# Performance work log

Measured on AMD Instinct MI355X. Metric: run time of the kernel, lower is better.

Reference implementation:

```python
import jax, jax.numpy as jnp
import numpy as np

KSIZE = 51  # radius=50 is even -> incremented to 51 in __init__


def _gaussian_1d(ksize):
    # cv2.getGaussianKernel with sigma<=0: sigma = 0.3*((ksize-1)*0.5 - 1) + 0.8
    sigma = 0.3 * ((ksize - 1) * 0.5 - 1) + 0.8
    x = np.arange(ksize, dtype=np.float64) - (ksize - 1) / 2
    g = np.exp(-(x * x) / (2.0 * sigma * sigma))
    g = g / g.sum()
    return g.astype(np.float32)


def _blur(img, kernel1d):
    """Separable Gaussian blur with reflect padding.
    Mathematically identical to the 2D conv with outer(g, g) in the torch code.
    img: (b, c, h, w), kernel1d: (k,)
    """
    k = kernel1d.shape[0]
    p = k // 2
    b, c, h, w = img.shape
    x = jnp.pad(img, ((0, 0), (0, 0), (p, p), (p, p)), mode='reflect')
    x = x.reshape(b * c, 1, h + 2 * p, w + 2 * p)
    # vertical pass then horizontal pass (conv vs correlation irrelevant: symmetric kernel)
    kv = kernel1d.reshape(1, 1, k, 1)
    kh = kernel1d.reshape(1, 1, 1, k)
    dn = ('NCHW', 'OIHW', 'NCHW')
    x = jax.lax.conv_general_dilated(x, kv, (1, 1), 'VALID', dimension_numbers=dn)
    x = jax.lax.conv_general_dilated(x, kh, (1, 1), 'VALID', dimension_numbers=dn)
    return x.reshape(b, c, h, w)


def setup_inputs() -> dict:
    key = jax.random.key(0)
    img = jax.random.uniform(key, (16, 3, 512, 512), dtype=jnp.float32)
    kernel1d = jnp.asarray(_gaussian_1d(KSIZE))
    return {"img": img, "kernel1d": kernel1d}


def reference(img, kernel1d):
    weight = 0.5
    threshold = 10.0
    blur = _blur(img, kernel1d)
    residual = img - blur
    mask = (jnp.abs(residual) * 255.0 > threshold).astype(img.dtype)
    soft_mask = _blur(mask, kernel1d)
    sharp = jnp.clip(img + weight * residual, 0.0, 1.0)
    return soft_mask * sharp + (1.0 - soft_mask) * img
```

## Files before the change

### kernel.cpp

```cpp
#include <hip/hip_runtime.h>
#include <hip/hip_bf16.h>


typedef __attribute__((ext_vector_type(8))) short bf16x8;
typedef __attribute__((ext_vector_type(4))) float f32x4;

constexpr int IMG = 512, NIMG = 48, K = 51;
constexpr int SP = 136;
constexpr int YP = 136;
constexpr int SROWS = 128;
constexpr int SDATA = 122;

__device__ __forceinline__ float bf2f(unsigned short u) {
    return __builtin_bit_cast(float, (unsigned)u << 16);
}
__device__ __forceinline__ unsigned short f2bf(float f) {
    unsigned u = __builtin_bit_cast(unsigned, f);
    u += 0x7FFF + ((u >> 16) & 1);
    return (unsigned short)(u >> 16);
}
__device__ __forceinline__ int refl(int i) {
    i = i < 0 ? -i : i;
    return i >= IMG ? 2 * IMG - 2 - i : i;
}

template <int PASS>
__global__ __launch_bounds__(512, 6) void usm_kern(const float* __restrict__ img,
                                                   unsigned short* __restrict__ resbuf,
                                                   unsigned char* __restrict__ maskbuf,
                                                   float* __restrict__ out,
                                                   const float* __restrict__ k1d) {
    __shared__ unsigned short st[SROWS * SP];
    __shared__ unsigned short Hl[64 * YP];

    const int tid = threadIdx.x, lane = tid & 63;
    const int wv = __builtin_amdgcn_readfirstlane(tid >> 6);
    const int m16 = lane & 15, g = lane >> 4;

    const int id = blockIdx.x;
    const int sw = (id & 7) * 384 + (id >> 3);
    const int bz = sw >> 6, r6 = sw & 63, byy = r6 >> 3, bxx = r6 & 7;
    const int x0 = bxx * 64, y0 = byy * 64;
    const size_t base = (size_t)bz * (IMG * IMG);
    const float* __restrict__ imgb = img + base;
    unsigned short* __restrict__ resb = resbuf + base;
    unsigned char* __restrict__ maskb = maskbuf + base;
    float* __restrict__ outb = out + base;

    bf16x8 a_v[2], a_h[2];
#pragma unroll
    for (int rs = 0; rs < 2; ++rs) {
        float gt[9];
#pragma unroll
        for (int e = 0; e < 9; ++e) {
            const int t = 32 * rs + 8 * g + e - m16;
            gt[e] = ((unsigned)t < (unsigned)K) ? k1d[t] : 0.f;
        }
#pragma unroll
        for (int j = 0; j < 8; ++j) {
            a_v[rs][j] = (short)f2bf(gt[j]);
            a_h[rs][j] = (short)f2bf(gt[j + 1]);
        }
    }
    const float gg0 = k1d[0], gg49 = k1d[49], gg50 = k1d[50];

    const bool xedge = (bxx == 0) | (bxx == 7);
    const int r0t = tid >> 4, c8 = (tid & 15) * 8;
#pragma unroll
    for (int j = 0; j < 4; ++j) {
        const int s = r0t + 32 * j;
        const int rowo = refl(y0 - 33 + min(s, SDATA - 1)) * IMG + (x0 - 32 + c8);
        unsigned pk[4];
        if (PASS == 0) {
            float v[8];
            if (!xedge) {
                const f32x4 f0 = *(const f32x4*)&imgb[rowo];
                const f32x4 f1 = *(const f32x4*)&imgb[rowo + 4];
#pragma unroll
                for (int e = 0; e < 4; ++e) { v[e] = f0[e]; v[e + 4] = f1[e]; }
            } else {
                const int rb = rowo - (x0 - 32 + c8);
#pragma unroll
                for (int e = 0; e < 8; ++e) v[e] = imgb[rb + refl(x0 - 32 + c8 + e)];
            }
#pragma unroll
            for (int w = 0; w < 4; ++w)
                pk[w] = (unsigned)f2bf(v[2 * w]) | ((unsigned)f2bf(v[2 * w + 1]) << 16);
        } else {
            unsigned char mb[8];
            if (!xedge) {
                const uint2 mv = *(const uint2*)&maskb[rowo];
#pragma unroll
                for (int e = 0; e < 4; ++e) {
                    mb[e] = (unsigned char)(mv.x >> (8 * e));
                    mb[e + 4] = (unsigned char)(mv.y >> (8 * e));
                }
            } else {
                const int rb = rowo - (x0 - 32 + c8);
#pragma unroll
                for (int e = 0; e < 8; ++e) mb[e] = maskb[rb + refl(x0 - 32 + c8 + e)];
            }
#pragma unroll
            for (int w = 0; w < 4; ++w)
                pk[w] = (mb[2 * w] ? 0x3F80u : 0u) | ((mb[2 * w + 1] ? 0x3F80u : 0u) << 16);
        }
        *(uint4*)&st[s * SP + c8] = make_uint4(pk[0], pk[1], pk[2], pk[3]);
    }

    f32x4 ivp[2];
    uint2 rvp[2];
#pragma unroll
    for (int k2 = 0; k2 < 2; ++k2) {
        const int t = wv + 8 * k2;
        const int xs = t & 3, ys = t >> 2;
        const int di = (y0 + 16 * ys + m16) * IMG + (x0 + 16 * xs + 4 * g);
        ivp[k2] = *(const f32x4*)&imgb[di];
        if (PASS == 1) rvp[k2] = *(const uint2*)&resb[di];
    }
    __syncthreads();

#pragma unroll
    for (int k4 = 0; k4 < 4; ++k4) {
        const int t = wv + 8 * k4;
        const int xs = t & 3, yt = t >> 2;
        f32x4 acc = {0.f, 0.f, 0.f, 0.f};
#pragma unroll
        for (int rs = 0; rs < 2; ++rs) {
            const bf16x8 ad = *(const bf16x8*)&st[(16 * yt + m16) * SP + 16 * xs + 8 + 32 * rs + 8 * g];
            acc = __builtin_amdgcn_mfma_f32_16x16x32_bf16(ad, a_h[rs], acc, 0, 0, 0);
        }
        if (m16 == 0) {
#pragma unroll
            for (int q = 0; q < 4; ++q)
                acc[q] = fmaf(gg0, bf2f(st[(16 * yt + 4 * g + q) * SP + 16 * xs + 7]), acc[q]);
        }
        if (m16 == 15) {
#pragma unroll
            for (int q = 0; q < 4; ++q)
                acc[q] = fmaf(gg50, bf2f(st[(16 * yt + 4 * g + q) * SP + 16 * xs + 72]), acc[q]);
        }
        const unsigned lo = (unsigned)f2bf(acc[0]) | ((unsigned)f2bf(acc[1]) << 16);
        const unsigned hi = (unsigned)f2bf(acc[2]) | ((unsigned)f2bf(acc[3]) << 16);
        *(uint2*)&Hl[(16 * xs + m16) * YP + 16 * yt + 4 * g] = make_uint2(lo, hi);
    }
    __syncthreads();

#pragma unroll
    for (int k2 = 0; k2 < 2; ++k2) {
        const int t = wv + 8 * k2;
        const int xs = t & 3, ys = t >> 2;
        f32x4 acc = {0.f, 0.f, 0.f, 0.f};
#pragma unroll
        for (int rs = 0; rs < 2; ++rs) {
            const bf16x8 ah = *(const bf16x8*)&Hl[(16 * xs + m16) * YP + 16 * ys + 8 + 32 * rs + 8 * g];
            acc = __builtin_amdgcn_mfma_f32_16x16x32_bf16(ah, a_v[rs], acc, 0, 0, 0);
        }
        if (m16 == 14) {
#pragma unroll
            for (int q = 0; q < 4; ++q)
                acc[q] = fmaf(gg50, bf2f(Hl[(16 * xs + 4 * g + q) * YP + 16 * ys + 72]), acc[q]);
        }
        if (m16 == 15) {
#pragma unroll
            for (int q = 0; q < 4; ++q) {
                const int hb = (16 * xs + 4 * g + q) * YP + 16 * ys;
                acc[q] = fmaf(gg49, bf2f(Hl[hb + 72]), fmaf(gg50, bf2f(Hl[hb + 73]), acc[q]));
            }
        }
        const int di = (y0 + 16 * ys + m16) * IMG + (x0 + 16 * xs + 4 * g);
        const f32x4 iv = ivp[k2];
        if (PASS == 0) {
            unsigned mw = 0;
            unsigned rp[2];
            float rv[4];
#pragma unroll
            for (int q = 0; q < 4; ++q) {
                rv[q] = iv[q] - acc[q];
                mw |= (fabsf(rv[q]) * 255.0f > 10.0f ? 1u : 0u) << (8 * q);
            }
            rp[0] = (unsigned)f2bf(rv[0]) | ((unsigned)f2bf(rv[1]) << 16);
            rp[1] = (unsigned)f2bf(rv[2]) | ((unsigned)f2bf(rv[3]) << 16);
            *(uint2*)&resb[di] = make_uint2(rp[0], rp[1]);
            *(unsigned*)&maskb[di] = mw;
        } else {
            f32x4 o;
#pragma unroll
            for (int q = 0; q < 4; ++q) {
                const unsigned rw = (q < 2) ? rvp[k2].x : rvp[k2].y;
                const float rvq = bf2f((unsigned short)(rw >> ((q & 1) * 16)));
                float sharp = fmaf(0.5f, rvq, iv[q]);
                sharp = fminf(fmaxf(sharp, 0.f), 1.f);
                o[q] = fmaf(acc[q], sharp - iv[q], iv[q]);
            }
            *(f32x4*)&outb[di] = o;
        }
    }
}

extern "C" void kernel_launch(void* const* d_in, const int* in_sizes, int n_in,
                              void* d_out, int out_size, void* d_ws, size_t ws_size,
                              hipStream_t stream) {
    (void)in_sizes; (void)n_in; (void)out_size; (void)ws_size;
    const float* img = (const float*)d_in[0];
    const float* k1d = (const float*)d_in[1];
    float* out = (float*)d_out;
    unsigned short* rs = (unsigned short*)d_ws;
    unsigned char* mk = (unsigned char*)d_ws + (size_t)NIMG * IMG * IMG * 2;

    const dim3 grid(NIMG * 64);

    usm_kern<0><<<grid, 512, 0, stream>>>(img, rs, mk, out, k1d);
    usm_kern<1><<<grid, 512, 0, stream>>>(img, rs, mk, out, k1d);
}
```

Baseline: 113.1 us.

## Drop mask buffer, derive mask from bf16 residual, alias LDS tiles

Pass 0 no longer writes a separate byte mask. Pass 1 reads the bf16 residual halo and rebuilds the mask with an integer magnitude compare, which removes one global buffer write and read. The horizontal-pass LDS buffer now reuses the staging buffer, with an extra barrier, so LDS use shrinks and launch bounds rise to 8 blocks. Manual bf16 rounding is replaced by the packed v_cvt_pk_bf16_f32 instruction, and the MFMA operands are swapped so edge taps need fewer lanes. The risk is that the threshold test on a bf16-rounded residual can flip mask bits near the cutoff, and the transposed Hl writes become scalar 16-bit LDS stores.

Result: no change. 113.5 us (+0.3%).

```diff
diff --git a/kernel.cpp b/kernel.cpp
--- a/kernel.cpp
+++ b/kernel.cpp
@@ -14,10 +14,10 @@
 __device__ __forceinline__ float bf2f(unsigned short u) {
     return __builtin_bit_cast(float, (unsigned)u << 16);
 }
-__device__ __forceinline__ unsigned short f2bf(float f) {
-    unsigned u = __builtin_bit_cast(unsigned, f);
-    u += 0x7FFF + ((u >> 16) & 1);
-    return (unsigned short)(u >> 16);
+__device__ __forceinline__ unsigned cvtpk(float lo, float hi) {
+    unsigned r;
+    asm("v_cvt_pk_bf16_f32 %0, %1, %2" : "=v"(r) : "v"(lo), "v"(hi));
+    return r;
 }
 __device__ __forceinline__ int refl(int i) {
     i = i < 0 ? -i : i;
@@ -25,13 +25,12 @@
 }
 
 template <int PASS>
-__global__ __launch_bounds__(512, 6) void usm_kern(const float* __restrict__ img,
+__global__ __launch_bounds__(512, 8) void usm_kern(const float* __restrict__ img,
                                                    unsigned short* __restrict__ resbuf,
-                                                   unsigned char* __restrict__ maskbuf,
                                                    float* __restrict__ out,
                                                    const float* __restrict__ k1d) {
     __shared__ unsigned short st[SROWS * SP];
-    __shared__ unsigned short Hl[64 * YP];
+    unsigned short* const Hl = st;
 
     const int tid = threadIdx.x, lane = tid & 63;
     const int wv = __builtin_amdgcn_readfirstlane(tid >> 6);
@@ -44,7 +43,6 @@
     const size_t base = (size_t)bz * (IMG * IMG);
     const float* __restrict__ imgb = img + base;
     unsigned short* __restrict__ resb = resbuf + base;
-    unsigned char* __restrict__ maskb = maskbuf + base;
     float* __restrict__ outb = out + base;
 
     bf16x8 a_v[2], a_h[2];
@@ -56,11 +54,13 @@
             const int t = 32 * rs + 8 * g + e - m16;
             gt[e] = ((unsigned)t < (unsigned)K) ? k1d[t] : 0.f;
         }
-#pragma unroll
-        for (int j = 0; j < 8; ++j) {
-            a_v[rs][j] = (short)f2bf(gt[j]);
-            a_h[rs][j] = (short)f2bf(gt[j + 1]);
-        }
+        uint4 uv, uh;
+        uv.x = cvtpk(gt[0], gt[1]); uv.y = cvtpk(gt[2], gt[3]);
+        uv.z = cvtpk(gt[4], gt[5]); uv.w = cvtpk(gt[6], gt[7]);
+        uh.x = cvtpk(gt[1], gt[2]); uh.y = cvtpk(gt[3], gt[4]);
+        uh.z = cvtpk(gt[5], gt[6]); uh.w = cvtpk(gt[7], gt[8]);
+        a_v[rs] = __builtin_bit_cast(bf16x8, uv);
+        a_h[rs] = __builtin_bit_cast(bf16x8, uh);
     }
     const float gg0 = k1d[0], gg49 = k1d[49], gg50 = k1d[50];
 
@@ -84,25 +84,27 @@
                 for (int e = 0; e < 8; ++e) v[e] = imgb[rb + refl(x0 - 32 + c8 + e)];
             }
 #pragma unroll
-            for (int w = 0; w < 4; ++w)
-                pk[w] = (unsigned)f2bf(v[2 * w]) | ((unsigned)f2bf(v[2 * w + 1]) << 16);
+            for (int w = 0; w < 4; ++w) pk[w] = cvtpk(v[2 * w], v[2 * w + 1]);
         } else {
-            unsigned char mb[8];
+            unsigned rw[4];
             if (!xedge) {
-                const uint2 mv = *(const uint2*)&maskb[rowo];
-#pragma unroll
-                for (int e = 0; e < 4; ++e) {
-                    mb[e] = (unsigned char)(mv.x >> (8 * e));
-                    mb[e + 4] = (unsigned char)(mv.y >> (8 * e));
-                }
+                const uint4 q4 = *(const uint4*)&resb[rowo];
+                rw[0] = q4.x; rw[1] = q4.y; rw[2] = q4.z; rw[3] = q4.w;
             } else {
                 const int rb = rowo - (x0 - 32 + c8);
 #pragma unroll
-                for (int e = 0; e < 8; ++e) mb[e] = maskb[rb + refl(x0 - 32 + c8 + e)];
-            }
-#pragma unroll
-            for (int w = 0; w < 4; ++w)
-                pk[w] = (mb[2 * w] ? 0x3F80u : 0u) | ((mb[2 * w + 1] ? 0x3F80u : 0u) << 16);
+                for (int w = 0; w < 4; ++w) {
+                    const unsigned short e0 = resb[rb + refl(x0 - 32 + c8 + 2 * w)];
+                    const unsigned short e1 = resb[rb + refl(x0 - 32 + c8 + 2 * w + 1)];
+                    rw[w] = (unsigned)e0 | ((unsigned)e1 << 16);
+                }
+            }
+#pragma unroll
+            for (int w = 0; w < 4; ++w) {
+                const unsigned lo = ((rw[w] & 0x7FFFu) > 0x3D20u) ? 0x3F80u : 0u;
+                const unsigned hi = (((rw[w] >> 16) & 0x7FFFu) > 0x3D20u) ? 0x3F80u : 0u;
+                pk[w] = lo | (hi << 16);
+            }
         }
         *(uint4*)&st[s * SP + c8] = make_uint4(pk[0], pk[1], pk[2], pk[3]);
     }
@@ -119,29 +121,35 @@
     }
     __syncthreads();
 
+    f32x4 cacc[4];
 #pragma unroll
     for (int k4 = 0; k4 < 4; ++k4) {
         const int t = wv + 8 * k4;
         const int xs = t & 3, yt = t >> 2;
+        const int n = 16 * yt + m16;
         f32x4 acc = {0.f, 0.f, 0.f, 0.f};
 #pragma unroll
         for (int rs = 0; rs < 2; ++rs) {
-            const bf16x8 ad = *(const bf16x8*)&st[(16 * yt + m16) * SP + 16 * xs + 8 + 32 * rs + 8 * g];
-            acc = __builtin_amdgcn_mfma_f32_16x16x32_bf16(ad, a_h[rs], acc, 0, 0, 0);
-        }
-        if (m16 == 0) {
-#pragma unroll
-            for (int q = 0; q < 4; ++q)
-                acc[q] = fmaf(gg0, bf2f(st[(16 * yt + 4 * g + q) * SP + 16 * xs + 7]), acc[q]);
-        }
-        if (m16 == 15) {
-#pragma unroll
-            for (int q = 0; q < 4; ++q)
-                acc[q] = fmaf(gg50, bf2f(st[(16 * yt + 4 * g + q) * SP + 16 * xs + 72]), acc[q]);
-        }
-        const unsigned lo = (unsigned)f2bf(acc[0]) | ((unsigned)f2bf(acc[1]) << 16);
-        const unsigned hi = (unsigned)f2bf(acc[2]) | ((unsigned)f2bf(acc[3]) << 16);
-        *(uint2*)&Hl[(16 * xs + m16) * YP + 16 * yt + 4 * g] = make_uint2(lo, hi);
+            const bf16x8 b = *(const bf16x8*)&st[n * SP + 16 * xs + 8 + 32 * rs + 8 * g];
+            acc = __builtin_amdgcn_mfma_f32_16x16x32_bf16(a_h[rs], b, acc, 0, 0, 0);
+        }
+        if (g == 0) acc[0] = fmaf(gg0,  bf2f(st[n * SP + 16 * xs + 7]),  acc[0]);
+        if (g == 3) acc[3] = fmaf(gg50, bf2f(st[n * SP + 16 * xs + 72]), acc[3]);
+        cacc[k4] = acc;
+    }
+    __syncthreads();
+
+#pragma unroll
+    for (int k4 = 0; k4 < 4; ++k4) {
+        const int t = wv + 8 * k4;
+        const int xs = t & 3, yt = t >> 2;
+        const int n = 16 * yt + m16;
+        const unsigned u01 = cvtpk(cacc[k4][0], cacc[k4][1]);
+        const unsigned u23 = cvtpk(cacc[k4][2], cacc[k4][3]);
+        Hl[(16 * xs + 4 * g + 0) * YP + n] = (unsigned short)u01;
+        Hl[(16 * xs + 4 * g + 1) * YP + n] = (unsigned short)(u01 >> 16);
+        Hl[(16 * xs + 4 * g + 2) * YP + n] = (unsigned short)u23;
+        Hl[(16 * xs + 4 * g + 3) * YP + n] = (unsigned short)(u23 >> 16);
     }
     __syncthreads();
 
@@ -170,18 +178,10 @@
         const int di = (y0 + 16 * ys + m16) * IMG + (x0 + 16 * xs + 4 * g);
         const f32x4 iv = ivp[k2];
         if (PASS == 0) {
-            unsigned mw = 0;
-            unsigned rp[2];
             float rv[4];
 #pragma unroll
-            for (int q = 0; q < 4; ++q) {
-                rv[q] = iv[q] - acc[q];
-                mw |= (fabsf(rv[q]) * 255.0f > 10.0f ? 1u : 0u) << (8 * q);
-            }
-            rp[0] = (unsigned)f2bf(rv[0]) | ((unsigned)f2bf(rv[1]) << 16);
-            rp[1] = (unsigned)f2bf(rv[2]) | ((unsigned)f2bf(rv[3]) << 16);
-            *(uint2*)&resb[di] = make_uint2(rp[0], rp[1]);
-            *(unsigned*)&maskb[di] = mw;
+            for (int q = 0; q < 4; ++q) rv[q] = iv[q] - acc[q];
+            *(uint2*)&resb[di] = make_uint2(cvtpk(rv[0], rv[1]), cvtpk(rv[2], rv[3]));
         } else {
             f32x4 o;
 #pragma unroll
@@ -205,10 +205,9 @@
     const float* k1d = (const float*)d_in[1];
     float* out = (float*)d_out;
     unsigned short* rs = (unsigned short*)d_ws;
-    unsigned char* mk = (unsigned char*)d_ws + (size_t)NIMG * IMG * IMG * 2;
 
     const dim3 grid(NIMG * 64);
 
-    usm_kern<0><<<grid, 512, 0, stream>>>(img, rs, mk, out, k1d);
-    usm_kern<1><<<grid, 512, 0, stream>>>(img, rs, mk, out, k1d);
-}
+    usm_kern<0><<<grid, 512, 0, stream>>>(img, rs, out, k1d);
+    usm_kern<1><<<grid, 512, 0, stream>>>(img, rs, out, k1d);
+}
```
